# Kernel optimization log

Measured on AMD Instinct MI355X. Metric: run time of the kernel, lower is better.

## Reference

```python
import jax, jax.numpy as jnp
import numpy as np
import math

H = 1024
N_HEADS = 16
B, S = 2, 2048

def setup_inputs() -> dict:
    key = jax.random.key(0)
    ks = jax.random.split(key, 10)
    s = 0.02
    inp = {
        "x": jax.random.normal(ks[0], (B, S, H), dtype=jnp.float32),
        "attention_mask": jnp.zeros((B, 1, 1, S), dtype=jnp.float32),
        "Wq": jax.random.normal(ks[1], (H, H), dtype=jnp.float32) * s,
        "bq": jnp.zeros((H,), dtype=jnp.float32),
        "Wk": jax.random.normal(ks[2], (H, H), dtype=jnp.float32) * s,
        "bk": jnp.zeros((H,), dtype=jnp.float32),
        "Wv": jax.random.normal(ks[3], (H, H), dtype=jnp.float32) * s,
        "bv": jnp.zeros((H,), dtype=jnp.float32),
        "Wo": jax.random.normal(ks[4], (H, H), dtype=jnp.float32) * s,
        "bo": jnp.zeros((H,), dtype=jnp.float32),
    }
    return inp

def reference(x, attention_mask, Wq, bq, Wk, bk, Wv, bv, Wo, bo):
    b, s, h = x.shape
    n = N_HEADS
    d = h // n
    scale = 1.0 / math.sqrt(h / n)
    # Linear projections (torch Linear: x @ W.T + b)
    q = (x @ Wq.T + bq).reshape(b, s, n, d).transpose(0, 2, 1, 3)  # [b,n,s,d]
    k = (x @ Wk.T + bk).reshape(b, s, n, d).transpose(0, 2, 1, 3)
    v = (x @ Wv.T + bv).reshape(b, s, n, d).transpose(0, 2, 1, 3)
    scores = jnp.einsum("bnqd,bnkd->bnqk", q, k) * scale + attention_mask
    probs = jax.nn.softmax(scores, axis=-1)
    attn = jnp.einsum("bnqk,bnkd->bnqd", probs, v)
    attn = attn.transpose(0, 2, 1, 3).reshape(b, s, h)
    return attn @ Wo.T + bo
```

## Files before the change

kernel.cpp:

```cpp
#include <hip/hip_runtime.h>

typedef __bf16 bf16;
typedef __bf16 bf16x8 __attribute__((ext_vector_type(8)));
typedef __bf16 bf16x4 __attribute__((ext_vector_type(4)));
typedef float f32x4 __attribute__((ext_vector_type(4)));
typedef float f32x16 __attribute__((ext_vector_type(16)));
typedef unsigned int u32;
typedef u32 u32x4 __attribute__((ext_vector_type(4)));
typedef const u32 __attribute__((address_space(1)))* gp1_t;
typedef u32 __attribute__((address_space(3)))* lp3_t;

constexpr int Hdim = 1024;
constexpr int SEQ  = 2048;
constexpr int NB   = 2;
constexpr int NHEAD = 16;
constexpr int DHEAD = 64;
constexpr int MR = NB * SEQ;
constexpr float LOG2E = 1.4426950408889634f;
constexpr float QSCALE = 0.125f * LOG2E;

__device__ __forceinline__ float fexp2(float x) { return __builtin_amdgcn_exp2f(x); }

__device__ __forceinline__ void gld16(const void* g, void* l) {
  __builtin_amdgcn_global_load_lds((gp1_t)g, (lp3_t)l, 16, 0, 0);
}

__device__ __forceinline__ u32 cvtpk_bf16(float lo, float hi) {
  u32 r;
  asm("v_cvt_pk_bf16_f32 %0, %1, %2" : "=v"(r) : "v"(lo), "v"(hi));
  return r;
}

__global__ __launch_bounds__(256) void cvt_all_k(
    const float* __restrict__ x, const float* __restrict__ Wq, const float* __restrict__ Wk,
    const float* __restrict__ Wv, const float* __restrict__ Wo, const float* __restrict__ mask,
    bf16* __restrict__ xb, bf16* __restrict__ wqkv, bf16* __restrict__ wob,
    float* __restrict__ maskS) {
  const int n8x = MR * Hdim / 8;
  const int n8w = Hdim * Hdim / 8;
  int i = blockIdx.x * 256 + threadIdx.x;
  if (i >= n8x + 4 * n8w) {
    int o = i - (n8x + 4 * n8w);
    const float4* p = reinterpret_cast<const float4*>(mask) + (size_t)o * 2;
    float4 a = p[0], b = p[1];
    a.x *= LOG2E; a.y *= LOG2E; a.z *= LOG2E; a.w *= LOG2E;
    b.x *= LOG2E; b.y *= LOG2E; b.z *= LOG2E; b.w *= LOG2E;
    float4* q = reinterpret_cast<float4*>(maskS) + (size_t)o * 2;
    q[0] = a; q[1] = b;
    return;
  }
  const float* src;
  bf16* dst;
  int slot;
  if (i < n8x) {
    src = x; dst = xb; slot = i;
  } else {
    int j = i - n8x;
    int w = j >> 17;
    int o = j & (n8w - 1);
    if (w == 0)      { src = Wq; dst = wqkv;            }
    else if (w == 1) { src = Wk; dst = wqkv + (size_t)Hdim * Hdim;     }
    else if (w == 2) { src = Wv; dst = wqkv + (size_t)2 * Hdim * Hdim; }
    else             { src = Wo; dst = wob;             }
    slot = o;
  }
  const float4* p = reinterpret_cast<const float4*>(src) + (size_t)slot * 2;
  float4 a = p[0], b = p[1];
  bf16x8 o8;
  o8[0] = (bf16)a.x; o8[1] = (bf16)a.y; o8[2] = (bf16)a.z; o8[3] = (bf16)a.w;
  o8[4] = (bf16)b.x; o8[5] = (bf16)b.y; o8[6] = (bf16)b.z; o8[7] = (bf16)b.w;
  reinterpret_cast<bf16x8*>(dst)[slot] = o8;
}

__global__ __launch_bounds__(256) void qkv_gemm_k(
    const bf16* __restrict__ A, const bf16* __restrict__ Bw,
    const float* __restrict__ bq, const float* __restrict__ bk, const float* __restrict__ bv,
    bf16* __restrict__ Qw, bf16* __restrict__ Kw, bf16* __restrict__ VTw)
{
  __shared__ __align__(16) bf16 As[3][128][32];
  __shared__ __align__(16) bf16 Bs[3][128][32];

  const int t = threadIdx.x;
  const int lane = t & 63, wave = t >> 6;
  const int ql = lane & 15, g = lane >> 4;
  const int wr = wave >> 1, wc = wave & 1;
  const int row0 = blockIdx.x * 128;
  const int col0 = blockIdx.y * 128;
  const int z = blockIdx.y >> 3;
  const float* bias = (z == 0) ? bq : (z == 1) ? bk : bv;

  f32x4 acc[4][4] = {};

#define STAGE_QKV(buf, kt)                                                        \
  {                                                                               \
    _Pragma("unroll")                                                             \
    for (int i = 0; i < 2; ++i) {                                                 \
      int c = i * 256 + t;                                                        \
      int r = c >> 2, o = (c & 3) << 3;                                           \
      gld16(&A[(size_t)(row0 + r) * Hdim + (kt) + o], (char*)&As[buf][0][0] + c * 16); \
      gld16(&Bw[(size_t)(col0 + r) * Hdim + (kt) + o], (char*)&Bs[buf][0][0] + c * 16); \
    }                                                                             \
  }

  constexpr int NT = Hdim / 32;
  STAGE_QKV(0, 0);
  STAGE_QKV(1, 32);

  int cur = 0;
  for (int it = 0; it < NT; ++it) {
    if (it + 2 < NT) {
      int stg = cur + 2; if (stg >= 3) stg -= 3;
      STAGE_QKV(stg, (it + 2) * 32);
      asm volatile("s_waitcnt vmcnt(8)" ::: "memory");
    } else if (it + 1 < NT) {
      asm volatile("s_waitcnt vmcnt(4)" ::: "memory");
    } else {
      asm volatile("s_waitcnt vmcnt(0)" ::: "memory");
    }
    __builtin_amdgcn_s_barrier();

    bf16x8 af[4], bfr[4];
#pragma unroll
    for (int m = 0; m < 4; ++m)
      af[m] = *reinterpret_cast<const bf16x8*>(&As[cur][wr * 64 + m * 16 + ql][g * 8]);
#pragma unroll
    for (int n = 0; n < 4; ++n)
      bfr[n] = *reinterpret_cast<const bf16x8*>(&Bs[cur][wc * 64 + n * 16 + ql][g * 8]);
#pragma unroll
    for (int m = 0; m < 4; ++m)
#pragma unroll
      for (int n = 0; n < 4; ++n)
        acc[m][n] = __builtin_amdgcn_mfma_f32_16x16x32_bf16(af[m], bfr[n], acc[m][n], 0, 0, 0);

    __builtin_amdgcn_s_barrier();
    cur = (cur + 1 == 3) ? 0 : cur + 1;
  }
#undef STAGE_QKV

  const float oscale = (z == 0) ? QSCALE : 1.0f;
#pragma unroll
  for (int m = 0; m < 4; ++m) {
#pragma unroll
    for (int n = 0; n < 4; ++n) {
#pragma unroll
      for (int r = 0; r < 4; ++r) {
        int gi = row0 + wr * 64 + m * 16 + g * 4 + r;
        int gj = col0 + wc * 64 + n * 16 + ql;
        int j1 = gj & (Hdim - 1);
        float v = (acc[m][n][r] + bias[j1]) * oscale;
        int b = gi >> 11, s = gi & (SEQ - 1);
        int hh = j1 >> 6, dd = j1 & 63;
        if (z == 0)
          Qw[((size_t)(b * NHEAD + hh) * SEQ + s) * DHEAD + dd] = (bf16)v;
        else if (z == 1)
          Kw[((size_t)(b * NHEAD + hh) * SEQ + s) * DHEAD + dd] = (bf16)v;
        else
          VTw[((size_t)(b * NHEAD + hh) * DHEAD + dd) * SEQ + s] = (bf16)v;
      }
    }
  }
}

__global__ __launch_bounds__(256, 3) void attn_fwd_k(
    const bf16* __restrict__ Q, const bf16* __restrict__ K,
    const bf16* __restrict__ VT, const float* __restrict__ maskS,
    bf16* __restrict__ Out)
{
  const int head = blockIdx.x;
  const int qt = blockIdx.y;
  const int b = head >> 4;
  const int hh = head & 15;
  const int t = threadIdx.x, lane = t & 63, wave = t >> 6;
  const int q = lane & 31, h = lane >> 5;

  __shared__ __align__(16) bf16 Ks[2][64][64];
  __shared__ __align__(16) bf16 VTs[2][64][64];

  const bf16* Qh  = Q  + (size_t)head * SEQ * DHEAD;
  const bf16* Kh  = K  + (size_t)head * SEQ * DHEAD;
  const bf16* VTh = VT + (size_t)head * DHEAD * SEQ;
  const float* mrow = maskS + (size_t)b * SEQ;

  const int q0w = qt * 128 + wave * 32;

  bf16x8 qf[4];
#pragma unroll
  for (int s = 0; s < 4; ++s)
    qf[s] = *reinterpret_cast<const bf16x8*>(&Qh[(size_t)(q0w + q) * DHEAD + s * 16 + 8 * h]);

  f32x16 accT[2] = {};
  f32x4 psum4 = {0.f, 0.f, 0.f, 0.f};

#pragma unroll
  for (int i = 0; i < 2; ++i) {
    int c = i * 256 + t, r = c >> 3, sp = c & 7, sl = sp ^ (r & 7);
    gld16(&Kh[(size_t)r * DHEAD + sl * 8], (char*)&Ks[0][0][0] + c * 16);
    gld16(&VTh[(size_t)r * SEQ + sl * 8], (char*)&VTs[0][0][0] + c * 16);
  }
  __syncthreads();

  for (int it = 0; it < SEQ / 64; ++it) {
    const int cur = it & 1;
    const int kb0 = it * 64;

    if (it + 1 < SEQ / 64) {
      const int nb0 = kb0 + 64;
#pragma unroll
      for (int i = 0; i < 2; ++i) {
        int c = i * 256 + t, r = c >> 3, sp = c & 7, sl = sp ^ (r & 7);
        gld16(&Kh[(size_t)(nb0 + r) * DHEAD + sl * 8], (char*)&Ks[cur ^ 1][0][0] + c * 16);
        gld16(&VTh[(size_t)r * SEQ + nb0 + sl * 8], (char*)&VTs[cur ^ 1][0][0] + c * 16);
      }
    }

    const char* ksb = (const char*)&Ks[cur][0][0];
    const char* vsb = (const char*)&VTs[cur][0][0];

    f32x16 sacc[2];
#pragma unroll
    for (int tt = 0; tt < 2; ++tt) {
#pragma unroll
      for (int s = 0; s < 4; ++s) {
        f32x4 m4 = *reinterpret_cast<const f32x4*>(mrow + kb0 + 32 * tt + 8 * s + 4 * h);
#pragma unroll
        for (int r = 0; r < 4; ++r) sacc[tt][s * 4 + r] = m4[r];
      }
    }

    __builtin_amdgcn_s_setprio(1);
#pragma unroll
    for (int tt = 0; tt < 2; ++tt) {
      const int row = 32 * tt + q;
      const int rsw = (row & 7) << 4;
#pragma unroll
      for (int s = 0; s < 4; ++s) {
        bf16x8 kf = *reinterpret_cast<const bf16x8*>(ksb + row * 128 + ((32 * s + 16 * h) ^ rsw));
        sacc[tt] = __builtin_amdgcn_mfma_f32_32x32x16_bf16(kf, qf[s], sacc[tt], 0, 0, 0);
      }
    }
    __builtin_amdgcn_s_setprio(0);

    float pe[2][16];
#pragma unroll
    for (int tt = 0; tt < 2; ++tt)
#pragma unroll
      for (int i = 0; i < 16; ++i) {
        pe[tt][i] = fexp2(sacc[tt][i]);
        psum4[i & 3] += pe[tt][i];
      }

    u32x4 pw[4];
#pragma unroll
    for (int m = 0; m < 4; ++m) {
      const int tt = m >> 1, mi = (m & 1) * 8;
      u32 w0a = cvtpk_bf16(pe[tt][mi + 0], pe[tt][mi + 1]);
      u32 w0b = cvtpk_bf16(pe[tt][mi + 2], pe[tt][mi + 3]);
      u32 w1a = cvtpk_bf16(pe[tt][mi + 4], pe[tt][mi + 5]);
      u32 w1b = cvtpk_bf16(pe[tt][mi + 6], pe[tt][mi + 7]);
      asm("v_permlane32_swap_b32 %0, %1" : "+v"(w0a), "+v"(w1a));
      asm("v_permlane32_swap_b32 %0, %1" : "+v"(w0b), "+v"(w1b));
      pw[m][0] = w0a; pw[m][1] = w0b; pw[m][2] = w1a; pw[m][3] = w1b;
    }

    __builtin_amdgcn_s_setprio(1);
#pragma unroll
    for (int td = 0; td < 2; ++td) {
      const int row = 32 * td + q;
      const int rsw = (row & 7) << 4;
#pragma unroll
      for (int m = 0; m < 4; ++m) {
        bf16x8 vf = *reinterpret_cast<const bf16x8*>(vsb + row * 128 + ((32 * m + 16 * h) ^ rsw));
        bf16x8 pf = __builtin_bit_cast(bf16x8, pw[m]);
        accT[td] = __builtin_amdgcn_mfma_f32_32x32x16_bf16(vf, pf, accT[td], 0, 0, 0);
      }
    }
    __builtin_amdgcn_s_setprio(0);

    __syncthreads();
  }

  float l = (psum4[0] + psum4[1]) + (psum4[2] + psum4[3]);
  l += __shfl_xor(l, 32);
  const float inv = 1.0f / l;

  char* slab = (char*)&Ks[0][0][0] + wave * 4096;
  const int qsw = (q & 7) << 4;
#pragma unroll
  for (int td = 0; td < 2; ++td)
#pragma unroll
    for (int s = 0; s < 4; ++s) {
      bf16x4 o4;
#pragma unroll
      for (int r = 0; r < 4; ++r) o4[r] = (bf16)(accT[td][s * 4 + r] * inv);
      *reinterpret_cast<bf16x4*>(slab + q * 128 + (((32 * td + 8 * s + 4 * h) * 2) ^ qsw)) = o4;
    }
  asm volatile("s_waitcnt lgkmcnt(0)" ::: "memory");
#pragma unroll
  for (int i = 0; i < 4; ++i) {
    const int row = i * 8 + (lane >> 3);
    bf16x8 v = *reinterpret_cast<const bf16x8*>(slab + row * 128 + (((lane & 7) << 4) ^ ((row & 7) << 4)));
    *reinterpret_cast<bf16x8*>(&Out[((size_t)(b * SEQ) + q0w + row) * Hdim + hh * 64 + (lane & 7) * 8]) = v;
  }
}

__global__ __launch_bounds__(256) void out_gemm_k(
    const bf16* __restrict__ A, const bf16* __restrict__ Bm,
    const float* __restrict__ bias, float* __restrict__ C)
{
  __shared__ __align__(16) bf16 As[3][128][32];
  __shared__ __align__(16) bf16 Bs[3][64][32];

  const int t = threadIdx.x;
  const int lane = t & 63, wave = t >> 6;
  const int ql = lane & 15, g = lane >> 4;
  const int wr = wave >> 1, wc = wave & 1;
  const int row0 = blockIdx.x * 128;
  const int col0 = blockIdx.y * 64;

  f32x4 acc[4][2] = {};

#define STAGE_OUT(buf, kt)                                                        \
  {                                                                               \
    _Pragma("unroll")                                                             \
    for (int i = 0; i < 2; ++i) {                                                 \
      int c = i * 256 + t;                                                        \
      int r = c >> 2, o = (c & 3) << 3;                                           \
      gld16(&A[(size_t)(row0 + r) * Hdim + (kt) + o], (char*)&As[buf][0][0] + c * 16); \
    }                                                                             \
    {                                                                             \
      int c = t;                                                                  \
      int r = c >> 2, o = (c & 3) << 3;                                           \
      gld16(&Bm[(size_t)(col0 + r) * Hdim + (kt) + o], (char*)&Bs[buf][0][0] + c * 16); \
    }                                                                             \
  }

  constexpr int NT = Hdim / 32;
  STAGE_OUT(0, 0);
  STAGE_OUT(1, 32);

  int cur = 0;
  for (int it = 0; it < NT; ++it) {
    if (it + 2 < NT) {
      int stg = cur + 2; if (stg >= 3) stg -= 3;
      STAGE_OUT(stg, (it + 2) * 32);
      asm volatile("s_waitcnt vmcnt(6)" ::: "memory");
    } else if (it + 1 < NT) {
      asm volatile("s_waitcnt vmcnt(3)" ::: "memory");
    } else {
      asm volatile("s_waitcnt vmcnt(0)" ::: "memory");
    }
    __builtin_amdgcn_s_barrier();

    bf16x8 af[4], bfr[2];
#pragma unroll
    for (int m = 0; m < 4; ++m)
      af[m] = *reinterpret_cast<const bf16x8*>(&As[cur][wr * 64 + m * 16 + ql][g * 8]);
#pragma unroll
    for (int n = 0; n < 2; ++n)
      bfr[n] = *reinterpret_cast<const bf16x8*>(&Bs[cur][wc * 32 + n * 16 + ql][g * 8]);
#pragma unroll
    for (int m = 0; m < 4; ++m)
#pragma unroll
      for (int n = 0; n < 2; ++n)
        acc[m][n] = __builtin_amdgcn_mfma_f32_16x16x32_bf16(af[m], bfr[n], acc[m][n], 0, 0, 0);

    __builtin_amdgcn_s_barrier();
    cur = (cur + 1 == 3) ? 0 : cur + 1;
  }
#undef STAGE_OUT

#pragma unroll
  for (int m = 0; m < 4; ++m)
#pragma unroll
    for (int n = 0; n < 2; ++n)
#pragma unroll
      for (int r = 0; r < 4; ++r) {
        int gi = row0 + wr * 64 + m * 16 + g * 4 + r;
        int gj = col0 + wc * 32 + n * 16 + ql;
        C[(size_t)gi * Hdim + gj] = acc[m][n][r] + bias[gj];
      }
}

extern "C" void kernel_launch(void* const* d_in, const int* in_sizes, int n_in,
                              void* d_out, int out_size, void* d_ws, size_t ws_size,
                              hipStream_t stream) {
  const float* x    = (const float*)d_in[0];
  const float* mask = (const float*)d_in[1];
  const float* Wq   = (const float*)d_in[2];
  const float* bq   = (const float*)d_in[3];
  const float* Wk   = (const float*)d_in[4];
  const float* bk   = (const float*)d_in[5];
  const float* Wv   = (const float*)d_in[6];
  const float* bv   = (const float*)d_in[7];
  const float* Wo   = (const float*)d_in[8];
  const float* bo   = (const float*)d_in[9];
  float* out = (float*)d_out;

  bf16* xb   = (bf16*)d_ws;
  const size_t big = (size_t)MR * Hdim;
  bf16* wqkv = xb + big;
  bf16* wob  = wqkv + (size_t)3 * Hdim * Hdim;
  bf16* qw   = wob + (size_t)Hdim * Hdim;
  bf16* kw   = qw + big;
  bf16* vtw  = kw + big;
  bf16* attnb = vtw + big;
  float* maskS = (float*)(attnb + big);

  const int nslots = MR * Hdim / 8 + 4 * (Hdim * Hdim / 8) + NB * SEQ / 8;
  cvt_all_k<<<nslots / 256, 256, 0, stream>>>(x, Wq, Wk, Wv, Wo, mask, xb, wqkv, wob, maskS);

  qkv_gemm_k<<<dim3(MR / 128, 3 * Hdim / 128), 256, 0, stream>>>(
      xb, wqkv, bq, bk, bv, qw, kw, vtw);

  attn_fwd_k<<<dim3(NB * NHEAD, SEQ / 128), 256, 0, stream>>>(qw, kw, vtw, maskS, attnb);

  out_gemm_k<<<dim3(MR / 128, Hdim / 64), 256, 0, stream>>>(attnb, wob, bo, out);
}
```

Before: 123.0 us.

## Replace triple-buffered QKV GEMM pipeline with single-buffer BK=64 and XCD-aware block remap

Swaps the QKV projection GEMM's three-stage async-load pipeline (BK=32) for a single shared buffer with BK=64 that waits for every load before computing. It also remaps block IDs so consecutive blocks land on the same XCD group and share L2-resident tiles. The intent is fewer barriers per K step and better L2 locality across chiplets. The cost is that global loads no longer overlap with MFMA work, so load latency is exposed.

```diff
diff --git a/kernel.cpp b/kernel.cpp
--- a/kernel.cpp
+++ b/kernel.cpp
@@ -77,65 +77,52 @@
     const float* __restrict__ bq, const float* __restrict__ bk, const float* __restrict__ bv,
     bf16* __restrict__ Qw, bf16* __restrict__ Kw, bf16* __restrict__ VTw)
 {
-  __shared__ __align__(16) bf16 As[3][128][32];
-  __shared__ __align__(16) bf16 Bs[3][128][32];
+  __shared__ __align__(16) bf16 As[128][64];
+  __shared__ __align__(16) bf16 Bs[128][64];
 
   const int t = threadIdx.x;
   const int lane = t & 63, wave = t >> 6;
   const int ql = lane & 15, g = lane >> 4;
   const int wr = wave >> 1, wc = wave & 1;
-  const int row0 = blockIdx.x * 128;
-  const int col0 = blockIdx.y * 128;
-  const int z = blockIdx.y >> 3;
+
+  const int bid = blockIdx.y * 32 + blockIdx.x;
+  const int w = (bid & 7) * 96 + (bid >> 3);
+  const int bx = w & 31, by = w >> 5;
+  const int row0 = bx * 128;
+  const int col0 = by * 128;
+  const int z = by >> 3;
   const float* bias = (z == 0) ? bq : (z == 1) ? bk : bv;
 
   f32x4 acc[4][4] = {};
 
-#define STAGE_QKV(buf, kt)                                                        \
-  {                                                                               \
-    _Pragma("unroll")                                                             \
-    for (int i = 0; i < 2; ++i) {                                                 \
-      int c = i * 256 + t;                                                        \
-      int r = c >> 2, o = (c & 3) << 3;                                           \
-      gld16(&A[(size_t)(row0 + r) * Hdim + (kt) + o], (char*)&As[buf][0][0] + c * 16); \
-      gld16(&Bw[(size_t)(col0 + r) * Hdim + (kt) + o], (char*)&Bs[buf][0][0] + c * 16); \
-    }                                                                             \
-  }
-
-  constexpr int NT = Hdim / 32;
-  STAGE_QKV(0, 0);
-  STAGE_QKV(1, 32);
-
-  int cur = 0;
-  for (int it = 0; it < NT; ++it) {
-    if (it + 2 < NT) {
-      int stg = cur + 2; if (stg >= 3) stg -= 3;
-      STAGE_QKV(stg, (it + 2) * 32);
-      asm volatile("s_waitcnt vmcnt(8)" ::: "memory");
-    } else if (it + 1 < NT) {
-      asm volatile("s_waitcnt vmcnt(4)" ::: "memory");
-    } else {
-      asm volatile("s_waitcnt vmcnt(0)" ::: "memory");
-    }
-    __builtin_amdgcn_s_barrier();
-
-    bf16x8 af[4], bfr[4];
-#pragma unroll
-    for (int m = 0; m < 4; ++m)
-      af[m] = *reinterpret_cast<const bf16x8*>(&As[cur][wr * 64 + m * 16 + ql][g * 8]);
-#pragma unroll
-    for (int n = 0; n < 4; ++n)
-      bfr[n] = *reinterpret_cast<const bf16x8*>(&Bs[cur][wc * 64 + n * 16 + ql][g * 8]);
-#pragma unroll
-    for (int m = 0; m < 4; ++m)
+  for (int kt = 0; kt < Hdim; kt += 64) {
+    __syncthreads();
+#pragma unroll
+    for (int i = 0; i < 4; ++i) {
+      int c = i * 256 + t;
+      int r = c >> 3, o = (c & 7) << 3;
+      gld16(&A[(size_t)(row0 + r) * Hdim + kt + o], (char*)&As[0][0] + c * 16);
+      gld16(&Bw[(size_t)(col0 + r) * Hdim + kt + o], (char*)&Bs[0][0] + c * 16);
+    }
+    asm volatile("s_waitcnt vmcnt(0)" ::: "memory");
+    __syncthreads();
+
+#pragma unroll
+    for (int kk = 0; kk < 2; ++kk) {
+      bf16x8 af[4], bfr[4];
+#pragma unroll
+      for (int m = 0; m < 4; ++m)
+        af[m] = *reinterpret_cast<const bf16x8*>(&As[wr * 64 + m * 16 + ql][kk * 32 + g * 8]);
 #pragma unroll
       for (int n = 0; n < 4; ++n)
-        acc[m][n] = __builtin_amdgcn_mfma_f32_16x16x32_bf16(af[m], bfr[n], acc[m][n], 0, 0, 0);
-
-    __builtin_amdgcn_s_barrier();
-    cur = (cur + 1 == 3) ? 0 : cur + 1;
-  }
-#undef STAGE_QKV
+        bfr[n] = *reinterpret_cast<const bf16x8*>(&Bs[wc * 64 + n * 16 + ql][kk * 32 + g * 8]);
+#pragma unroll
+      for (int m = 0; m < 4; ++m)
+#pragma unroll
+        for (int n = 0; n < 4; ++n)
+          acc[m][n] = __builtin_amdgcn_mfma_f32_16x16x32_bf16(af[m], bfr[n], acc[m][n], 0, 0, 0);
+    }
+  }
 
   const float oscale = (z == 0) ? QSCALE : 1.0f;
 #pragma unroll
@@ -409,7 +396,7 @@
   const int nslots = MR * Hdim / 8 + 4 * (Hdim * Hdim / 8) + NB * SEQ / 8;
   cvt_all_k<<<nslots / 256, 256, 0, stream>>>(x, Wq, Wk, Wv, Wo, mask, xb, wqkv, wob, maskS);
 
-  qkv_gemm_k<<<dim3(MR / 128, 3 * Hdim / 128), 256, 0, stream>>>(
+  qkv_gemm_k<<<dim3(32, 24), 256, 0, stream>>>(
       xb, wqkv, bq, bk, bv, qw, kw, vtw);
 
   attn_fwd_k<<<dim3(NB * NHEAD, SEQ / 128), 256, 0, stream>>>(qw, kw, vtw, maskS, attnb);
```

Measured after the change: 147.7 us. 1.2x slower.

## Swizzle GEMM LDS tiles and triple-buffer attention K/V with LDS mask

Applied to the files above, without the earlier changes.

The QKV and output GEMMs now XOR-swizzle the 16-byte chunks in their LDS tiles, on both the global-to-LDS loads and the fragment reads, to cut LDS bank conflicts. The attention kernel moves from double to triple buffering of K/V tiles with explicit vmcnt waits and one barrier per iteration, replacing the full __syncthreads. It also preloads the whole mask row into LDS instead of reading it from global memory each iteration. The extra LDS (about 56KB per block) forces the occupancy hint down from 3 to 2 blocks per CU, which may cost latency hiding.

```diff
diff --git a/kernel.cpp b/kernel.cpp
--- a/kernel.cpp
+++ b/kernel.cpp
@@ -88,6 +88,7 @@
   const int col0 = blockIdx.y * 128;
   const int z = blockIdx.y >> 3;
   const float* bias = (z == 0) ? bq : (z == 1) ? bk : bv;
+  const int rsl = (g ^ ((ql >> 1) & 3)) * 8;
 
   f32x4 acc[4][4] = {};
 
@@ -96,9 +97,10 @@
     _Pragma("unroll")                                                             \
     for (int i = 0; i < 2; ++i) {                                                 \
       int c = i * 256 + t;                                                        \
-      int r = c >> 2, o = (c & 3) << 3;                                           \
-      gld16(&A[(size_t)(row0 + r) * Hdim + (kt) + o], (char*)&As[buf][0][0] + c * 16); \
-      gld16(&Bw[(size_t)(col0 + r) * Hdim + (kt) + o], (char*)&Bs[buf][0][0] + c * 16); \
+      int r = c >> 2, sp = c & 3;                                                 \
+      int sl = (sp ^ ((r >> 1) & 3)) << 3;                                        \
+      gld16(&A[(size_t)(row0 + r) * Hdim + (kt) + sl], (char*)&As[buf][0][0] + c * 16); \
+      gld16(&Bw[(size_t)(col0 + r) * Hdim + (kt) + sl], (char*)&Bs[buf][0][0] + c * 16); \
     }                                                                             \
   }
 
@@ -122,10 +124,10 @@
     bf16x8 af[4], bfr[4];
 #pragma unroll
     for (int m = 0; m < 4; ++m)
-      af[m] = *reinterpret_cast<const bf16x8*>(&As[cur][wr * 64 + m * 16 + ql][g * 8]);
+      af[m] = *reinterpret_cast<const bf16x8*>(&As[cur][wr * 64 + m * 16 + ql][rsl]);
 #pragma unroll
     for (int n = 0; n < 4; ++n)
-      bfr[n] = *reinterpret_cast<const bf16x8*>(&Bs[cur][wc * 64 + n * 16 + ql][g * 8]);
+      bfr[n] = *reinterpret_cast<const bf16x8*>(&Bs[cur][wc * 64 + n * 16 + ql][rsl]);
 #pragma unroll
     for (int m = 0; m < 4; ++m)
 #pragma unroll
@@ -161,7 +163,7 @@
   }
 }
 
-__global__ __launch_bounds__(256, 3) void attn_fwd_k(
+__global__ __launch_bounds__(256, 2) void attn_fwd_k(
     const bf16* __restrict__ Q, const bf16* __restrict__ K,
     const bf16* __restrict__ VT, const float* __restrict__ maskS,
     bf16* __restrict__ Out)
@@ -173,8 +175,9 @@
   const int t = threadIdx.x, lane = t & 63, wave = t >> 6;
   const int q = lane & 31, h = lane >> 5;
 
-  __shared__ __align__(16) bf16 Ks[2][64][64];
-  __shared__ __align__(16) bf16 VTs[2][64][64];
+  __shared__ __align__(16) bf16 Ks[3][64][64];
+  __shared__ __align__(16) bf16 VTs[3][64][64];
+  __shared__ __align__(16) float Ms[SEQ];
 
   const bf16* Qh  = Q  + (size_t)head * SEQ * DHEAD;
   const bf16* Kh  = K  + (size_t)head * SEQ * DHEAD;
@@ -191,37 +194,45 @@
   f32x16 accT[2] = {};
   f32x4 psum4 = {0.f, 0.f, 0.f, 0.f};
 
+#define STAGE_KV(buf, tile)                                                       \
+  {                                                                               \
+    const int nb0 = (tile) * 64;                                                  \
+    _Pragma("unroll")                                                             \
+    for (int i = 0; i < 2; ++i) {                                                 \
+      int c = i * 256 + t, r = c >> 3, sp = c & 7, sl = sp ^ (r & 7);             \
+      gld16(&Kh[(size_t)(nb0 + r) * DHEAD + sl * 8], (char*)&Ks[buf][0][0] + c * 16); \
+      gld16(&VTh[(size_t)r * SEQ + nb0 + sl * 8], (char*)&VTs[buf][0][0] + c * 16);   \
+    }                                                                             \
+  }
+
+  constexpr int NT = SEQ / 64;
 #pragma unroll
   for (int i = 0; i < 2; ++i) {
-    int c = i * 256 + t, r = c >> 3, sp = c & 7, sl = sp ^ (r & 7);
-    gld16(&Kh[(size_t)r * DHEAD + sl * 8], (char*)&Ks[0][0][0] + c * 16);
-    gld16(&VTh[(size_t)r * SEQ + sl * 8], (char*)&VTs[0][0][0] + c * 16);
-  }
-  __syncthreads();
-
-  for (int it = 0; it < SEQ / 64; ++it) {
-    const int cur = it & 1;
-    const int kb0 = it * 64;
-
-    if (it + 1 < SEQ / 64) {
-      const int nb0 = kb0 + 64;
-#pragma unroll
-      for (int i = 0; i < 2; ++i) {
-        int c = i * 256 + t, r = c >> 3, sp = c & 7, sl = sp ^ (r & 7);
-        gld16(&Kh[(size_t)(nb0 + r) * DHEAD + sl * 8], (char*)&Ks[cur ^ 1][0][0] + c * 16);
-        gld16(&VTh[(size_t)r * SEQ + nb0 + sl * 8], (char*)&VTs[cur ^ 1][0][0] + c * 16);
-      }
+    int c = i * 256 + t;
+    gld16(&mrow[c * 4], (char*)&Ms[0] + c * 16);
+  }
+  STAGE_KV(0, 0);
+  STAGE_KV(1, 1);
+  asm volatile("s_waitcnt vmcnt(4)" ::: "memory");
+  __builtin_amdgcn_s_barrier();
+
+  int cur = 0;
+  for (int it = 0; it < NT; ++it) {
+    if (it + 2 < NT) {
+      int stg = cur + 2; if (stg >= 3) stg -= 3;
+      STAGE_KV(stg, it + 2);
     }
 
     const char* ksb = (const char*)&Ks[cur][0][0];
     const char* vsb = (const char*)&VTs[cur][0][0];
+    const int kb0 = it * 64;
 
     f32x16 sacc[2];
 #pragma unroll
     for (int tt = 0; tt < 2; ++tt) {
 #pragma unroll
       for (int s = 0; s < 4; ++s) {
-        f32x4 m4 = *reinterpret_cast<const f32x4*>(mrow + kb0 + 32 * tt + 8 * s + 4 * h);
+        f32x4 m4 = *reinterpret_cast<const f32x4*>(&Ms[kb0 + 32 * tt + 8 * s + 4 * h]);
 #pragma unroll
         for (int r = 0; r < 4; ++r) sacc[tt][s * 4 + r] = m4[r];
       }
@@ -276,8 +287,12 @@
     }
     __builtin_amdgcn_s_setprio(0);
 
-    __syncthreads();
-  }
+    if (it + 2 < NT)      asm volatile("s_waitcnt vmcnt(4)" ::: "memory");
+    else if (it + 1 < NT) asm volatile("s_waitcnt vmcnt(0)" ::: "memory");
+    __builtin_amdgcn_s_barrier();
+    cur = (cur + 1 == 3) ? 0 : cur + 1;
+  }
+#undef STAGE_KV
 
   float l = (psum4[0] + psum4[1]) + (psum4[2] + psum4[3]);
   l += __shfl_xor(l, 32);
@@ -316,6 +331,7 @@
   const int wr = wave >> 1, wc = wave & 1;
   const int row0 = blockIdx.x * 128;
   const int col0 = blockIdx.y * 64;
+  const int rsl = (g ^ ((ql >> 1) & 3)) * 8;
 
   f32x4 acc[4][2] = {};
 
@@ -324,13 +340,15 @@
     _Pragma("unroll")                                                             \
     for (int i = 0; i < 2; ++i) {                                                 \
       int c = i * 256 + t;                                                        \
-      int r = c >> 2, o = (c & 3) << 3;                                           \
-      gld16(&A[(size_t)(row0 + r) * Hdim + (kt) + o], (char*)&As[buf][0][0] + c * 16); \
+      int r = c >> 2, sp = c & 3;                                                 \
+      int sl = (sp ^ ((r >> 1) & 3)) << 3;                                        \
+      gld16(&A[(size_t)(row0 + r) * Hdim + (kt) + sl], (char*)&As[buf][0][0] + c * 16); \
     }                                                                             \
     {                                                                             \
       int c = t;                                                                  \
-      int r = c >> 2, o = (c & 3) << 3;                                           \
-      gld16(&Bm[(size_t)(col0 + r) * Hdim + (kt) + o], (char*)&Bs[buf][0][0] + c * 16); \
+      int r = c >> 2, sp = c & 3;                                                 \
+      int sl = (sp ^ ((r >> 1) & 3)) << 3;                                        \
+      gld16(&Bm[(size_t)(col0 + r) * Hdim + (kt) + sl], (char*)&Bs[buf][0][0] + c * 16); \
     }                                                                             \
   }
 
@@ -354,10 +372,10 @@
     bf16x8 af[4], bfr[2];
 #pragma unroll
     for (int m = 0; m < 4; ++m)
-      af[m] = *reinterpret_cast<const bf16x8*>(&As[cur][wr * 64 + m * 16 + ql][g * 8]);
+      af[m] = *reinterpret_cast<const bf16x8*>(&As[cur][wr * 64 + m * 16 + ql][rsl]);
 #pragma unroll
     for (int n = 0; n < 2; ++n)
-      bfr[n] = *reinterpret_cast<const bf16x8*>(&Bs[cur][wc * 32 + n * 16 + ql][g * 8]);
+      bfr[n] = *reinterpret_cast<const bf16x8*>(&Bs[cur][wc * 32 + n * 16 + ql][rsl]);
 #pragma unroll
     for (int m = 0; m < 4; ++m)
 #pragma unroll
```

Result: faster. 118.2 us, median of 3 (-3.9%).
